# Kernel optimization log

Hardware: AMD Instinct MI355X
Metric: run time of the kernel (lower is better)

The kernel has to match this reference:

```python
import jax, jax.numpy as jnp
import numpy as np
from jax import lax

STRIDE = 16
SCALE = 16.0
ANCHOR_DIMS = (1.0, 2.0, 4.0, 8.0, 16.0, 32.0)
PRE_NMS_TOP_N = 6000
POST_NMS_TOP_N = 300
NMS_THRESH = 0.7


def conv2d(x, w, b, pad):
    y = lax.conv_general_dilated(x, w, (1, 1), [(pad, pad), (pad, pad)],
                                 dimension_numbers=("NCHW", "OIHW", "NCHW"))
    return y + b[None, :, None, None]


def setup_inputs() -> dict:
    key = jax.random.key(0)
    ks = jax.random.split(key, 6)
    B, C, H, W = 1, 1024, 128, 128
    A = len(ANCHOR_DIMS)
    return {
        "base_features": jax.random.normal(ks[0], (B, C, H, W), jnp.float32),
        "image_metadata": jnp.array([[H * STRIDE, W * STRIDE, 1.0]], jnp.float32),
        "gt_boxes": jax.random.uniform(ks[1], (B, 20, 5), jnp.float32) * 100.0,
        "W_conv": jax.random.normal(ks[2], (512, C, 3, 3), jnp.float32) / np.sqrt(C * 9.0),
        "b_conv": jnp.zeros((512,), jnp.float32),
        "W_cls": jax.random.normal(ks[3], (A, 512, 1, 1), jnp.float32) / np.sqrt(512.0),
        "b_cls": jnp.zeros((A,), jnp.float32),
        "W_bbox": jax.random.normal(ks[4], (4 * A, 512, 1, 1), jnp.float32) * 0.01,
        "b_bbox": jnp.zeros((4 * A,), jnp.float32),
    }


def _make_anchors(H, W):
    # square anchors of size dim*scale, centered on each feature cell
    dims = jnp.asarray(ANCHOR_DIMS, jnp.float32) * SCALE          # [A]
    cy = (jnp.arange(H, dtype=jnp.float32) + 0.5) * STRIDE        # [H]
    cx = (jnp.arange(W, dtype=jnp.float32) + 0.5) * STRIDE        # [W]
    half = 0.5 * dims[None, None, :]                              # [1,1,A]
    CX = cx[None, :, None]
    CY = cy[:, None, None]
    anchors = jnp.stack(jnp.broadcast_arrays(CX - half, CY - half, CX + half, CY + half), axis=-1)
    return anchors.reshape(-1, 4)                                 # [(H*W*A),4], order (h,w,a)


def _nms_fixed(boxes, scores):
    # boxes [N,4] already sorted by score desc; greedy NMS, POST_NMS_TOP_N picks
    x1, y1, x2, y2 = boxes[:, 0], boxes[:, 1], boxes[:, 2], boxes[:, 3]
    areas = jnp.maximum(x2 - x1, 0.0) * jnp.maximum(y2 - y1, 0.0)

    def body(i, state):
        alive, keep = state
        masked = jnp.where(alive, scores, -jnp.inf)
        j = jnp.argmax(masked)
        valid = masked[j] > -jnp.inf
        keep = keep.at[i].set(jnp.where(valid, j, -1).astype(jnp.int32))
        bj = boxes[j]
        iw = jnp.maximum(jnp.minimum(x2, bj[2]) - jnp.maximum(x1, bj[0]), 0.0)
        ih = jnp.maximum(jnp.minimum(y2, bj[3]) - jnp.maximum(y1, bj[1]), 0.0)
        inter = iw * ih
        iou = inter / (areas + areas[j] - inter + 1e-9)
        alive = alive & (iou <= NMS_THRESH)
        return alive, keep

    alive0 = jnp.ones(boxes.shape[0], bool)
    keep0 = jnp.full((POST_NMS_TOP_N,), -1, jnp.int32)
    _, keep = lax.fori_loop(0, POST_NMS_TOP_N, body, (alive0, keep0))
    return keep


def _proposal(prob, bbox, image_metadata):
    # original layer operates on detached tensors (.data)
    prob = lax.stop_gradient(prob)
    bbox = lax.stop_gradient(bbox)
    B, A, H, W = prob.shape
    anchors = _make_anchors(H, W)                                 # [N,4]
    scores = prob[0].transpose(1, 2, 0).reshape(-1)               # (h,w,a)
    deltas = bbox[0].reshape(A, 4, H, W).transpose(2, 3, 0, 1).reshape(-1, 4)
    wa = anchors[:, 2] - anchors[:, 0]
    ha = anchors[:, 3] - anchors[:, 1]
    cxa = anchors[:, 0] + 0.5 * wa
    cya = anchors[:, 1] + 0.5 * ha
    pcx = deltas[:, 0] * wa + cxa
    pcy = deltas[:, 1] * ha + cya
    pw = jnp.exp(deltas[:, 2]) * wa
    ph = jnp.exp(deltas[:, 3]) * ha
    boxes = jnp.stack([pcx - 0.5 * pw, pcy - 0.5 * ph, pcx + 0.5 * pw, pcy + 0.5 * ph], axis=1)
    im_h, im_w = image_metadata[0, 0], image_metadata[0, 1]
    boxes = jnp.stack([
        jnp.clip(boxes[:, 0], 0.0, im_w), jnp.clip(boxes[:, 1], 0.0, im_h),
        jnp.clip(boxes[:, 2], 0.0, im_w), jnp.clip(boxes[:, 3], 0.0, im_h)], axis=1)
    top_scores, top_idx = lax.top_k(scores, PRE_NMS_TOP_N)
    top_boxes = boxes[top_idx]
    keep = _nms_fixed(top_boxes, top_scores)
    sel = jnp.where(keep >= 0, keep, 0)
    kept = top_boxes[sel] * (keep >= 0).astype(top_boxes.dtype)[:, None]
    rois = jnp.concatenate([jnp.zeros((POST_NMS_TOP_N, 1), top_boxes.dtype), kept], axis=1)
    return rois                                                   # [POST_NMS_TOP_N, 5]


def reference(base_features, image_metadata, gt_boxes, W_conv, b_conv, W_cls, b_cls, W_bbox, b_bbox):
    conv1 = jax.nn.relu(conv2d(base_features, W_conv, b_conv, pad=1))   # [B,512,H,W]
    score = conv2d(conv1, W_cls, b_cls, pad=0)                          # [B,A,H,W]
    B, A, H, W = score.shape
    s2 = score.reshape(B, 2, (A * H) // 2, W)                           # RPN.reshape(x, 2)
    prob = jax.nn.softmax(s2, axis=1).reshape(B, A, H, W)               # reshape back to A channels
    bbox = conv2d(conv1, W_bbox, b_bbox, pad=0)                         # [B,4A,H,W]
    rois = _proposal(prob, bbox, image_metadata)
    return rois, prob, bbox
```

## Files before the change

kernel.cpp:

```cpp
#include <hip/hip_runtime.h>
#include <math.h>

typedef unsigned int u32;
typedef unsigned long long u64;
typedef short s16x8 __attribute__((ext_vector_type(8)));
typedef float f32x4 __attribute__((ext_vector_type(4)));

#define HH 128
#define WW 128
#define NPIX (128*128)
#define NANCH (NPIX*6)
#define KPRE 6000
#define KPOST 300
#define SORT_CAP 16384
#define RW 96
#define NMS_T 0.7f

#define OUT_PROB 1500
#define OUT_BBOX (1500 + 98304)

#define WS_CONV1 ((size_t)0)
#define WS_XTH   ((size_t)33554432)
#define WS_WPH   ((size_t)100663296)
#define WS_BOXES ((size_t)33554432)
#define WS_SCORE (WS_BOXES + 1572864)
#define WS_KEYS  (WS_SCORE + 393216)
#define WS_TB    (WS_KEYS + 131072)
#define WS_AREA  (WS_TB + 98304)
#define WS_SUP   (WS_AREA + 24576)
#define WS_HIST  (WS_SUP + 4718592)
#define WS_CTRL  (WS_HIST + 262144)
#define WS_KEEP  (WS_CTRL + 256)

__device__ __forceinline__ unsigned short f2bf(float x) {
    u32 b = __float_as_uint(x);
    u32 r = (b + 0x7FFFu + ((b >> 16) & 1u)) >> 16;
    return (unsigned short)r;
}

__device__ __forceinline__ void gl_lds16(const void* g, void* l) {
    __builtin_amdgcn_global_load_lds(
        (__attribute__((address_space(1))) const void*)g,
        (__attribute__((address_space(3))) void*)l,
        16, 0, 0);
}

__global__ void k_init(u32* __restrict__ hist, u32* __restrict__ ctrl,
                       int* __restrict__ keep, u64* __restrict__ keys) {
    int t = blockIdx.x * blockDim.x + threadIdx.x;
    if (t < 65536) hist[t] = 0u;
    if (t < 64)    ctrl[t] = 0u;
    if (t < 304)   keep[t] = -1;
    if (t < SORT_CAP) keys[t] = ~0ULL;
}

__global__ __launch_bounds__(256) void k_xsplit(const float* __restrict__ in,
                                                unsigned short* __restrict__ xth) {
    unsigned short* xtl = xth + 16777216;
    __shared__ unsigned short Th[64][72];
    __shared__ unsigned short Tl[64][72];
    const int px0 = blockIdx.x * 64;
    const int c0  = blockIdx.y * 64;
    const int t = threadIdx.x;
    const int r = t >> 4;
    const int p4 = (t & 15) * 4;
#pragma unroll
    for (int i = 0; i < 4; ++i) {
        int cr = r + 16 * i;
        float4 v = *(const float4*)(in + (size_t)(c0 + cr) * NPIX + px0 + p4);
        float vv[4] = {v.x, v.y, v.z, v.w};
#pragma unroll
        for (int k = 0; k < 4; ++k) {
            unsigned short h = f2bf(vv[k]);
            float hf = __uint_as_float((u32)h << 16);
            unsigned short l = f2bf(vv[k] - hf);
            Th[p4 + k][cr] = h;
            Tl[p4 + k][cr] = l;
        }
    }
    __syncthreads();
    const int p = t >> 2, q = t & 3;
    unsigned short* dh = xth + (size_t)(px0 + p) * 1024 + c0 + q * 16;
    unsigned short* dl = xtl + (size_t)(px0 + p) * 1024 + c0 + q * 16;
    *(uint4*)dh       = *(const uint4*)&Th[p][q * 16];
    *(uint4*)(dh + 8) = *(const uint4*)&Th[p][q * 16 + 8];
    *(uint4*)dl       = *(const uint4*)&Tl[p][q * 16];
    *(uint4*)(dl + 8) = *(const uint4*)&Tl[p][q * 16 + 8];
}

__global__ __launch_bounds__(256) void k_wpack(const float* __restrict__ w,
                                               unsigned short* __restrict__ wph,
                                               float* __restrict__ zstash) {
    if (blockIdx.x == 0 && threadIdx.x < 128) zstash[threadIdx.x] = 0.f;
    int id = blockIdx.x * 256 + threadIdx.x;
    int oc = id >> 10, c = id & 1023;
    const float* src = w + (size_t)oc * 9216 + c * 9;
#pragma unroll
    for (int tap = 0; tap < 9; ++tap) {
        float x = src[tap];
        unsigned short h = f2bf(x);
        unsigned short l = f2bf(x - __uint_as_float((u32)h << 16));
        wph[(size_t)tap * 524288 + id] = h;
        wph[4718592 + (size_t)tap * 524288 + id] = l;
    }
}

__global__ __launch_bounds__(256, 2) void k_conv3m(const unsigned short* __restrict__ xt,
                                                   const unsigned short* __restrict__ wp,
                                                   const float* __restrict__ bias,
                                                   const unsigned short* __restrict__ zst,
                                                   float* __restrict__ out) {
    const int bid = blockIdx.x;
    const int xcd = bid & 7;
    const int kk  = bid >> 3;
    const int ocg = kk & 3;
    const int y   = xcd * 16 + (kk >> 2);
    const int oc0 = ocg * 128;
    const int tid = threadIdx.x;
    const int lane = tid & 63;
    const int w    = tid >> 6;
    const int l15  = lane & 15;
    const int quad = lane >> 4;
    const int hoc  = w >> 1, hpx = w & 1;

    __shared__ __align__(16) unsigned short Lds[32768];

    const int lg  = lane & 3;
    const int lr  = lane >> 2;

    const unsigned short* xsrc[4];
    int xstep[4];
    const unsigned short* wsrc[4];

    int wp_pl[4], wp_ocr[4], wp_gs[4];
#pragma unroll
    for (int j = 0; j < 4; ++j) {
        int i = w + 4 * j;
        wp_pl[j]  = i >> 3;
        wp_ocr[j] = (i & 7) * 16 + lr;
        wp_gs[j]  = lg ^ ((wp_ocr[j] >> 1) & 3);
    }
    int xp_pl[4], xp_p[4], xp_gs[4];
#pragma unroll
    for (int j = 0; j < 4; ++j) {
        int i = w + 4 * j;
        xp_pl[j] = i >> 3;
        xp_p[j]  = (i & 7) * 16 + lr;
        xp_gs[j] = lg ^ ((xp_p[j] >> 1) & 3);
    }

    auto set_tap = [&](int tap) {
        int dy = tap / 3, dx = tap - dy * 3;
        int yy = y + dy - 1;
        bool yok = (yy >= 0) && (yy < HH);
#pragma unroll
        for (int j = 0; j < 4; ++j) {
            int x = dx - 1 + xp_p[j];
            bool ok = yok && (x >= 0) && (x < WW);
            xsrc[j] = ok ? xt + (size_t)xp_pl[j] * 16777216
                              + (size_t)(yy * WW + x) * 1024 + xp_gs[j] * 8
                         : zst + lg * 8;
            xstep[j] = ok ? 32 : 0;
        }
#pragma unroll
        for (int j = 0; j < 4; ++j)
            wsrc[j] = wp + (size_t)wp_pl[j] * 4718592 + (size_t)tap * 524288
                        + (size_t)(oc0 + wp_ocr[j]) * 1024 + wp_gs[j] * 8;
    };

    auto issue = [&](int sel) {
        const int bo = sel * 16384;
#pragma unroll
        for (int j = 0; j < 4; ++j) {
            gl_lds16(xsrc[j], &Lds[bo + (w + 4 * j) * 512]);
            xsrc[j] += xstep[j];
        }
#pragma unroll
        for (int j = 0; j < 4; ++j) {
            gl_lds16(wsrc[j], &Lds[bo + 8192 + (w + 4 * j) * 512]);
            wsrc[j] += 32;
        }
    };

    const int g  = quad ^ ((l15 >> 1) & 3);
    const int bB0 = (hpx * 64 + l15) * 32 + g * 8;
    const int bA0 = 8192 + (hoc * 64 + l15) * 32 + g * 8;

    f32x4 acc[4][4];
#pragma unroll
    for (int og = 0; og < 4; ++og)
#pragma unroll
        for (int nt = 0; nt < 4; ++nt) acc[og][nt] = (f32x4){0.f, 0.f, 0.f, 0.f};

    set_tap(0);
    issue(0);

    for (int s = 0; s < 288; ++s) {
        const int cur = s & 1;
        __syncthreads();
        if (s + 1 < 288) {
            int s1 = s + 1;
            if ((s1 & 31) == 0) set_tap(s1 >> 5);
            issue(s1 & 1);
        }

        const int bo = cur * 16384;
        s16x8 ah[4], al[4];
#pragma unroll
        for (int og = 0; og < 4; ++og) {
            ah[og] = *(const s16x8*)&Lds[bo + bA0 + og * 512];
            al[og] = *(const s16x8*)&Lds[bo + bA0 + 4096 + og * 512];
        }
#pragma unroll
        for (int nt = 0; nt < 4; ++nt) {
            const s16x8 bh = *(const s16x8*)&Lds[bo + bB0 + nt * 512];
            const s16x8 bl = *(const s16x8*)&Lds[bo + bB0 + 4096 + nt * 512];
#pragma unroll
            for (int og = 0; og < 4; ++og) {
                acc[og][nt] = __builtin_amdgcn_mfma_f32_16x16x32_bf16(ah[og], bh, acc[og][nt], 0, 0, 0);
                acc[og][nt] = __builtin_amdgcn_mfma_f32_16x16x32_bf16(ah[og], bl, acc[og][nt], 0, 0, 0);
                acc[og][nt] = __builtin_amdgcn_mfma_f32_16x16x32_bf16(al[og], bh, acc[og][nt], 0, 0, 0);
            }
        }
    }

#pragma unroll
    for (int og = 0; og < 4; ++og) {
#pragma unroll
        for (int nt = 0; nt < 4; ++nt) {
#pragma unroll
            for (int rg = 0; rg < 4; ++rg) {
                const int oc = oc0 + hoc * 64 + og * 16 + quad * 4 + rg;
                const int px = hpx * 64 + nt * 16 + l15;
                float v = acc[og][nt][rg] + bias[oc];
                out[(size_t)oc * NPIX + y * WW + px] = fmaxf(v, 0.f);
            }
        }
    }
}

__global__ __launch_bounds__(256) void k_conv1(const float* __restrict__ conv1,
                                               const float* __restrict__ wcls,
                                               const float* __restrict__ bcls,
                                               const float* __restrict__ wbox,
                                               const float* __restrict__ bboxb,
                                               float* __restrict__ out) {
    const int tid = threadIdx.x;
    const int og = tid >> 4, pg = tid & 15;
    const int px0 = blockIdx.x * 64;
    __shared__ __align__(16) float Wl[32][32];
    __shared__ __align__(16) float Xl[32][64];
    __shared__ float Sc[6][64];

    float a0[4] = {0, 0, 0, 0}, a1[4] = {0, 0, 0, 0};

    for (int cc = 0; cc < 16; ++cc) {
        {
            int u = tid;
            int row = (u * 4) >> 5;
            int col = (u * 4) & 31;
            float4 v;
            if (row < 6)       v = *(const float4*)(wcls + row * 512 + cc * 32 + col);
            else if (row < 30) v = *(const float4*)(wbox + (row - 6) * 512 + cc * 32 + col);
            else               v = make_float4(0.f, 0.f, 0.f, 0.f);
            *(float4*)&Wl[row][col] = v;
        }
        for (int u = tid; u < 512; u += 256) {
            int row = (u * 4) >> 6, col = (u * 4) & 63;
            *(float4*)&Xl[row][col] =
                *(const float4*)(conv1 + (size_t)(cc * 32 + row) * NPIX + px0 + col);
        }
        __syncthreads();
#pragma unroll
        for (int cp = 0; cp < 32; ++cp) {
            const float4 x = *(const float4*)&Xl[cp][pg * 4];
            const float w0 = Wl[og][cp];
            const float w1 = Wl[og + 16][cp];
            a0[0] = fmaf(w0, x.x, a0[0]); a0[1] = fmaf(w0, x.y, a0[1]);
            a0[2] = fmaf(w0, x.z, a0[2]); a0[3] = fmaf(w0, x.w, a0[3]);
            a1[0] = fmaf(w1, x.x, a1[0]); a1[1] = fmaf(w1, x.y, a1[1]);
            a1[2] = fmaf(w1, x.z, a1[2]); a1[3] = fmaf(w1, x.w, a1[3]);
        }
        __syncthreads();
    }
    const int pxb = px0 + pg * 4;
    if (og < 6) {
        const float bc = bcls[og];
#pragma unroll
        for (int kk = 0; kk < 4; ++kk) Sc[og][pg * 4 + kk] = a0[kk] + bc;
    } else {
        const float bb = bboxb[og - 6];
#pragma unroll
        for (int kk = 0; kk < 4; ++kk)
            out[OUT_BBOX + (size_t)(og - 6) * NPIX + pxb + kk] = a0[kk] + bb;
    }
    if (og + 16 < 30) {
        const float bb = bboxb[og + 10];
#pragma unroll
        for (int kk = 0; kk < 4; ++kk)
            out[OUT_BBOX + (size_t)(og + 10) * NPIX + pxb + kk] = a1[kk] + bb;
    }
    __syncthreads();
    if (og < 6) {
        const int pa = og < 3 ? og + 3 : og - 3;
#pragma unroll
        for (int kk = 0; kk < 4; ++kk) {
            const float s = Sc[og][pg * 4 + kk], sp = Sc[pa][pg * 4 + kk];
            out[OUT_PROB + (size_t)og * NPIX + pxb + kk] = 1.0f / (1.0f + expf(sp - s));
        }
    }
}

__global__ void k_decode(const float* __restrict__ out, const float* __restrict__ meta,
                         float4* __restrict__ boxes, float* __restrict__ scores,
                         u32* __restrict__ hist) {
#pragma clang fp contract(off)
    int t = blockIdx.x * blockDim.x + threadIdx.x;
    if (t >= NANCH) return;
    int a = t >> 14;
    int pix = t & 16383;
    int yc = pix >> 7, xc = pix & 127;
    int n = pix * 6 + a;
    float sc = out[OUT_PROB + (size_t)a * NPIX + pix];
    float d0 = out[OUT_BBOX + (size_t)(a * 4 + 0) * NPIX + pix];
    float d1 = out[OUT_BBOX + (size_t)(a * 4 + 1) * NPIX + pix];
    float d2 = out[OUT_BBOX + (size_t)(a * 4 + 2) * NPIX + pix];
    float d3 = out[OUT_BBOX + (size_t)(a * 4 + 3) * NPIX + pix];
    const float dims = (float)(16 << a);
    const float cxa = (xc + 0.5f) * 16.f;
    const float cya = (yc + 0.5f) * 16.f;
    float pcx = d0 * dims + cxa;
    float pcy = d1 * dims + cya;
    float pw  = expf(d2) * dims;
    float ph  = expf(d3) * dims;
    float imh = meta[0], imw = meta[1];
    float x1 = fminf(fmaxf(pcx - 0.5f * pw, 0.f), imw);
    float y1 = fminf(fmaxf(pcy - 0.5f * ph, 0.f), imh);
    float x2 = fminf(fmaxf(pcx + 0.5f * pw, 0.f), imw);
    float y2 = fminf(fmaxf(pcy + 0.5f * ph, 0.f), imh);
    boxes[n] = make_float4(x1, y1, x2, y2);
    scores[n] = sc;
    atomicAdd(&hist[__float_as_uint(sc) >> 16], 1u);
}

__global__ void k_select(const u32* __restrict__ hist, u32* __restrict__ ctrl) {
    __shared__ u32 S[256];
    __shared__ u32 U[256];
    const int tid = threadIdx.x;
    u32 s = 0;
    for (int i = 0; i < 256; ++i) s += hist[tid * 256 + i];
    S[tid] = s;
    __syncthreads();
    if (tid == 0) {
        u32 acc = 0;
        for (int t2 = 255; t2 >= 0; --t2) { U[t2] = acc; acc += S[t2]; }
    }
    __syncthreads();
    if (U[tid] < KPRE && U[tid] + S[tid] >= KPRE) {
        u32 acc = U[tid];
        for (int b = tid * 256 + 255; b >= tid * 256; --b) {
            u32 h = hist[b];
            if (acc + h >= KPRE) { ctrl[1] = (u32)b; ctrl[2] = acc; break; }
            acc += h;
        }
    }
}

__global__ void k_compact(const float* __restrict__ scores, u32* __restrict__ ctrl,
                          u64* __restrict__ keys) {
    int t = blockIdx.x * blockDim.x + threadIdx.x;
    if (t >= NANCH) return;
    u32 bits = __float_as_uint(scores[t]);
    if ((bits >> 16) >= ctrl[1]) {
        u32 pos = atomicAdd(&ctrl[0], 1u);
        if (pos < SORT_CAP) keys[pos] = ((u64)(~bits) << 32) | (u32)t;
    }
}

__global__ __launch_bounds__(1024) void k_sort_local(u64* __restrict__ keys) {
    __shared__ u64 lds[8192];
    const int tid = threadIdx.x;
    u64* g = keys + blockIdx.x * 8192;
    for (int u = tid; u < 8192; u += 1024) lds[u] = g[u];
    __syncthreads();
    for (int k = 2; k <= 8192; k <<= 1) {
        for (int j = k >> 1; j > 0; j >>= 1) {
            for (int u = tid; u < 4096; u += 1024) {
                int i = ((u & ~(j - 1)) << 1) | (u & (j - 1));
                int l = i | j;
                bool up = (i & k) == 0;
                u64 x = lds[i], y2 = lds[l];
                if ((x > y2) == up) { lds[i] = y2; lds[l] = x; }
            }
            __syncthreads();
        }
    }
    for (int u = tid; u < 8192; u += 1024) g[u] = lds[u];
}

__global__ void k_mergegather(const u64* __restrict__ keys,
                              const float4* __restrict__ boxes,
                              float4* __restrict__ tb, float* __restrict__ areas) {
#pragma clang fp contract(off)
    int i = blockIdx.x * blockDim.x + threadIdx.x;
    if (i >= KPRE) return;
    const u64* A = keys;
    const u64* B = keys + 8192;
    int lo = i > 8192 ? i - 8192 : 0;
    int hi = i < 8192 ? i : 8192;
    while (lo < hi) {
        int a = (lo + hi) >> 1;
        if (A[a] < B[i - a - 1]) lo = a + 1; else hi = a;
    }
    int a = lo, b = i - lo;
    u64 va = (a < 8192) ? A[a] : ~0ULL;
    u64 vb = (b < 8192) ? B[b] : ~0ULL;
    u64 v = va < vb ? va : vb;
    u32 n = (u32)(v & 0xFFFFFFFFULL);
    float4 bx = boxes[n];
    tb[i] = bx;
    areas[i] = fmaxf(bx.z - bx.x, 0.f) * fmaxf(bx.w - bx.y, 0.f);
}

__global__ __launch_bounds__(256) void k_bitmap(const float4* __restrict__ tb,
                                                const float* __restrict__ areas,
                                                u64* __restrict__ suppr) {
#pragma clang fp contract(off)
    const int i = blockIdx.x;
    const int lane = threadIdx.x & 63;
    const int wv = threadIdx.x >> 6;
    const float4 bi = tb[i];
    const float ai = areas[i];
    const int w0 = i >> 6;
    for (int Wd = w0 + wv; Wd < RW; Wd += 4) {
        int j = Wd * 64 + lane;
        bool sup = false;
        if (j < KPRE) {
            float4 bj = tb[j];
            float iw = fmaxf(fminf(bi.z, bj.z) - fmaxf(bi.x, bj.x), 0.f);
            float ih = fmaxf(fminf(bi.w, bj.w) - fmaxf(bi.y, bj.y), 0.f);
            float inter = iw * ih;
            float denom = ((areas[j] + ai) - inter) + 1e-9f;
            sup = (inter / denom) > NMS_T;
        }
        u64 m = __ballot(sup);
        if (lane == 0) suppr[(size_t)i * RW + Wd] = m;
    }
}

__global__ void k_scan(const u64* __restrict__ suppr, int* __restrict__ keep) {
    const int lane = threadIdx.x;
    u64 a0 = (lane < 93) ? ~0ULL : (lane == 93 ? ((1ULL << 48) - 1) : 0ULL);
    const int w1 = lane + 64;
    u64 a1 = (w1 < 93) ? ~0ULL : (w1 == 93 ? ((1ULL << 48) - 1) : 0ULL);
    int kept = 0;
    int i = 0;
    while (kept < KPOST) {
        int wi = i >> 6;
        if (wi >= 94) break;
        u64 wvv = (wi < 64) ? __shfl(a0, wi) : __shfl(a1, wi - 64);
        wvv &= (~0ULL) << (i & 63);
        if (wvv == 0ULL) { i = (wi + 1) << 6; continue; }
        int b = __ffsll((long long)wvv) - 1;
        i = (wi << 6) + b;
        if (lane == 0) keep[kept] = i;
        kept++;
        const u64* row = suppr + (size_t)i * RW;
        u64 s0 = row[lane];
        u64 s1 = (lane + 64 < RW) ? row[lane + 64] : 0ULL;
        a0 &= ~s0;
        a1 &= ~s1;
        i++;
    }
}

__global__ void k_rois(const int* __restrict__ keep, const float4* __restrict__ tb,
                       float* __restrict__ out) {
    int r = blockIdx.x * blockDim.x + threadIdx.x;
    if (r >= KPOST) return;
    int k = keep[r];
    float4 b = make_float4(0.f, 0.f, 0.f, 0.f);
    if (k >= 0) b = tb[k];
    out[r * 5 + 0] = 0.f;
    out[r * 5 + 1] = b.x;
    out[r * 5 + 2] = b.y;
    out[r * 5 + 3] = b.z;
    out[r * 5 + 4] = b.w;
}

extern "C" void kernel_launch(void* const* d_in, const int* in_sizes, int n_in,
                              void* d_out, int out_size, void* d_ws, size_t ws_size,
                              hipStream_t stream) {
    (void)in_sizes; (void)n_in; (void)out_size; (void)ws_size;
    const float* x     = (const float*)d_in[0];
    const float* meta  = (const float*)d_in[1];
    const float* wc3   = (const float*)d_in[3];
    const float* bc3   = (const float*)d_in[4];
    const float* wcls  = (const float*)d_in[5];
    const float* bcls  = (const float*)d_in[6];
    const float* wbox  = (const float*)d_in[7];
    const float* bboxb = (const float*)d_in[8];
    float* out = (float*)d_out;
    char* ws = (char*)d_ws;

    float*  conv1  = (float*)(ws + WS_CONV1);
    float4* boxes  = (float4*)(ws + WS_BOXES);
    float*  scores = (float*)(ws + WS_SCORE);
    u64*    keys   = (u64*)(ws + WS_KEYS);
    float4* tb     = (float4*)(ws + WS_TB);
    float*  areas  = (float*)(ws + WS_AREA);
    u64*    suppr  = (u64*)(ws + WS_SUP);
    u32*    hist   = (u32*)(ws + WS_HIST);
    u32*    ctrl   = (u32*)(ws + WS_CTRL);
    int*    keep   = (int*)(ws + WS_KEEP);

    float* zstash = out;

    unsigned short* xth = (unsigned short*)(ws + WS_XTH);
    unsigned short* wph = (unsigned short*)(ws + WS_WPH);
    k_xsplit<<<dim3(256, 16), 256, 0, stream>>>(x, xth);
    k_wpack<<<2048, 256, 0, stream>>>(wc3, wph, zstash);
    k_conv3m<<<512, 256, 0, stream>>>(xth, wph, bc3,
                                      (const unsigned short*)zstash, conv1);

    k_init<<<256, 256, 0, stream>>>(hist, ctrl, keep, keys);
    k_conv1<<<256, 256, 0, stream>>>(conv1, wcls, bcls, wbox, bboxb, out);
    k_decode<<<384, 256, 0, stream>>>(out, meta, boxes, scores, hist);
    k_select<<<1, 256, 0, stream>>>(hist, ctrl);
    k_compact<<<384, 256, 0, stream>>>(scores, ctrl, keys);
    k_sort_local<<<2, 1024, 0, stream>>>(keys);
    k_mergegather<<<24, 256, 0, stream>>>(keys, boxes, tb, areas);
    k_bitmap<<<6000, 256, 0, stream>>>(tb, areas, suppr);
    k_scan<<<1, 64, 0, stream>>>(suppr, keep);
    k_rois<<<2, 256, 0, stream>>>(keep, tb, out);
}
```

Measured before the change: 891.6 us.

## Block greedy NMS scan by 64-box chunks using diagonal suppression words

The bitmap kernel now also writes each box's diagonal suppression word to a compact array. The scan walks 64-box chunks: it resolves keeps within a chunk by register shuffles of the prefetched diagonal words, then ORs the suppression rows of all kept boxes once per chunk. This removes the serialized dependent global row load per kept box on the single-wavefront critical path. Row loads are still issued per kept box, but they are batched after the in-chunk decisions rather than gating each next decision.

```diff
diff --git a/kernel.cpp b/kernel.cpp
--- a/kernel.cpp
+++ b/kernel.cpp
@@ -31,6 +31,7 @@
 #define WS_HIST  (WS_SUP + 4718592)
 #define WS_CTRL  (WS_HIST + 262144)
 #define WS_KEEP  (WS_CTRL + 256)
+#define WS_DIAG  (WS_KEEP + 1280)
 
 __device__ __forceinline__ unsigned short f2bf(float x) {
     u32 b = __float_as_uint(x);
@@ -424,7 +425,8 @@
 
 __global__ __launch_bounds__(256) void k_bitmap(const float4* __restrict__ tb,
                                                 const float* __restrict__ areas,
-                                                u64* __restrict__ suppr) {
+                                                u64* __restrict__ suppr,
+                                                u64* __restrict__ diag) {
 #pragma clang fp contract(off)
     const int i = blockIdx.x;
     const int lane = threadIdx.x & 63;
@@ -444,33 +446,50 @@
             sup = (inter / denom) > NMS_T;
         }
         u64 m = __ballot(sup);
-        if (lane == 0) suppr[(size_t)i * RW + Wd] = m;
-    }
-}
-
-__global__ void k_scan(const u64* __restrict__ suppr, int* __restrict__ keep) {
+        if (lane == 0) {
+            suppr[(size_t)i * RW + Wd] = m;
+            if (Wd == w0) diag[i] = m;
+        }
+    }
+}
+
+__global__ void k_scan(const u64* __restrict__ suppr, const u64* __restrict__ diag,
+                       int* __restrict__ keep) {
     const int lane = threadIdx.x;
     u64 a0 = (lane < 93) ? ~0ULL : (lane == 93 ? ((1ULL << 48) - 1) : 0ULL);
     const int w1 = lane + 64;
     u64 a1 = (w1 < 93) ? ~0ULL : (w1 == 93 ? ((1ULL << 48) - 1) : 0ULL);
     int kept = 0;
-    int i = 0;
-    while (kept < KPOST) {
-        int wi = i >> 6;
-        if (wi >= 94) break;
-        u64 wvv = (wi < 64) ? __shfl(a0, wi) : __shfl(a1, wi - 64);
-        wvv &= (~0ULL) << (i & 63);
-        if (wvv == 0ULL) { i = (wi + 1) << 6; continue; }
-        int b = __ffsll((long long)wvv) - 1;
-        i = (wi << 6) + b;
-        if (lane == 0) keep[kept] = i;
-        kept++;
-        const u64* row = suppr + (size_t)i * RW;
-        u64 s0 = row[lane];
-        u64 s1 = (lane + 64 < RW) ? row[lane + 64] : 0ULL;
-        a0 &= ~s0;
-        a1 &= ~s1;
-        i++;
+    u64 dv_cur = diag[lane];
+    for (int c = 0; c < 94 && kept < KPOST; ++c) {
+        u64 dv_nxt = (c < 93) ? diag[(size_t)(c + 1) * 64 + lane] : 0ULL;
+        u64 ac = (c < 64) ? (u64)__shfl((long long)a0, c)
+                          : (u64)__shfl((long long)a1, c - 64);
+        u64 m = ac;
+        u64 keptMask = 0;
+        while (m && kept < KPOST) {
+            int b = __ffsll((long long)m) - 1;
+            if (lane == 0) keep[kept] = (c << 6) + b;
+            kept++;
+            keptMask |= (1ULL << b);
+            u64 dv = (u64)__shfl((long long)dv_cur, b);
+            m &= ~dv;
+            m &= ~(1ULL << b);
+        }
+        if (keptMask && kept < KPOST + 64) {
+            u64 s0 = 0, s1 = 0;
+            u64 km = keptMask;
+            while (km) {
+                int b = __ffsll((long long)km) - 1;
+                km &= km - 1;
+                const u64* row = suppr + (size_t)((c << 6) + b) * RW;
+                u64 r0 = (lane > c) ? row[lane] : 0ULL;
+                u64 r1 = (w1 > c && w1 < 94) ? row[w1] : 0ULL;
+                s0 |= r0; s1 |= r1;
+            }
+            a0 &= ~s0; a1 &= ~s1;
+        }
+        dv_cur = dv_nxt;
     }
 }
 
@@ -513,6 +532,7 @@
     u32*    hist   = (u32*)(ws + WS_HIST);
     u32*    ctrl   = (u32*)(ws + WS_CTRL);
     int*    keep   = (int*)(ws + WS_KEEP);
+    u64*    diag   = (u64*)(ws + WS_DIAG);
 
     float* zstash = out;
 
@@ -530,7 +550,7 @@
     k_compact<<<384, 256, 0, stream>>>(scores, ctrl, keys);
     k_sort_local<<<2, 1024, 0, stream>>>(keys);
     k_mergegather<<<24, 256, 0, stream>>>(keys, boxes, tb, areas);
-    k_bitmap<<<6000, 256, 0, stream>>>(tb, areas, suppr);
-    k_scan<<<1, 64, 0, stream>>>(suppr, keep);
+    k_bitmap<<<6000, 256, 0, stream>>>(tb, areas, suppr, diag);
+    k_scan<<<1, 64, 0, stream>>>(suppr, diag, keep);
     k_rois<<<2, 256, 0, stream>>>(keep, tb, out);
 }
```

Measured after the change: 889.1 us. No clear change (-0.3%).
